# Kernel optimization log

Measured on AMD Instinct MI355X. Metric: run time of the kernel, lower is better.

Reference implementation:

```python
import jax, jax.numpy as jnp
import numpy as np

STEPS = 4
EMB = 128
HEADS = 3
NUM_GRAPHS = 64
NODES_PER = 64
N = NUM_GRAPHS * NODES_PER
E_SPARSE = N * 16
DATA_LENS = [NODES_PER] * NUM_GRAPHS


def _complete_edge_index(data_lens):
    # dense_to_sparse(complete_matrix) -> all (i,j) pairs within each block,
    # including self loops (diagonal of complete_matrix is 1).
    srcs, dsts = [], []
    start = 0
    for l in data_lens:
        idx = np.arange(start, start + l)
        srcs.append(np.repeat(idx, l))
        dsts.append(np.tile(idx, l))
        start += l
    return np.stack([np.concatenate(srcs), np.concatenate(dsts)]).astype(np.int32)


def leaky(x, slope=0.01):
    return jnp.where(x >= 0, x, slope * x)


def setup_inputs() -> dict:
    key = jax.random.key(0)
    ks = jax.random.split(key, 16)
    s = 0.05
    edge_complete = jnp.asarray(_complete_edge_index(DATA_LENS))
    # sparse edge_index: random edges within each graph
    src_local = jax.random.randint(ks[1], (E_SPARSE,), 0, NODES_PER)
    dst_local = jax.random.randint(ks[2], (E_SPARSE,), 0, NODES_PER)
    gid = jnp.repeat(jnp.arange(NUM_GRAPHS), E_SPARSE // NUM_GRAPHS) * NODES_PER
    edge_index = jnp.stack([src_local + gid, dst_local + gid]).astype(jnp.int32)
    batch_ind = jnp.repeat(jnp.arange(NUM_GRAPHS), NODES_PER).astype(jnp.int32)
    return {
        "x": jax.random.normal(ks[0], (N, EMB), jnp.float32),
        "edge_index": edge_index,
        "batch_ind": batch_ind,
        "edge_complete": edge_complete,
        "Wm": jax.random.normal(ks[3], (STEPS, EMB, EMB)) * s,
        "bm": jnp.zeros((STEPS, EMB)),
        "Wa": jax.random.normal(ks[4], (STEPS, 3 * EMB, EMB)) * s,
        "ba": jnp.zeros((STEPS, EMB)),
        "Wl": jax.random.normal(ks[5], (STEPS - 1, EMB, HEADS * EMB)) * s,
        "bl": jnp.zeros((STEPS - 1, HEADS * EMB)),
        "Wr": jax.random.normal(ks[6], (STEPS - 1, EMB, HEADS * EMB)) * s,
        "br": jnp.zeros((STEPS - 1, HEADS * EMB)),
        "att_w": jax.random.normal(ks[7], (STEPS - 1, HEADS, EMB)) * s,
        "att_bias": jnp.zeros((STEPS - 1, EMB)),
    }


def _graphnet(x, x_att, batch_ind, src, dst, Wm, bm, Wa, ba):
    # message: f_mess(x_j)  (edge_attr is None in this model)
    m = leaky(x[src] @ Wm + bm)                               # [E, D]
    agg = jax.ops.segment_max(m, dst, num_segments=x.shape[0])
    agg = jnp.where(jnp.isneginf(agg), 0.0, agg)              # PyG fills empty with 0
    xg = x_att[batch_ind]                                     # [N, D]
    z = jnp.concatenate([x, xg, agg], axis=1)                 # [N, 3D]
    return leaky(z @ Wa + ba) + x


def _gatv2(x, src, dst, Wl, bl, Wr, br, att, bias):
    n = x.shape[0]
    xl = (x @ Wl + bl).reshape(n, HEADS, EMB)                 # source transform
    xr = (x @ Wr + br).reshape(n, HEADS, EMB)                 # target transform
    e = leaky(xl[src] + xr[dst], 0.2)                         # [E, H, D]
    logits = jnp.einsum('ehd,hd->eh', e, att)                 # [E, H]
    mx = jax.ops.segment_max(logits, dst, num_segments=n)
    mx = jnp.where(jnp.isneginf(mx), 0.0, mx)
    alpha = jnp.exp(logits - mx[dst])
    denom = jax.ops.segment_sum(alpha, dst, num_segments=n)
    alpha = alpha / denom[dst]                                # softmax over incoming edges
    out = jax.ops.segment_sum(alpha[:, :, None] * xl[src], dst, num_segments=n)
    return out.mean(axis=1) + bias                            # concat=False -> head mean


def reference(x, edge_index, batch_ind, edge_complete, Wm, bm, Wa, ba, Wl, bl, Wr, br, att_w, att_bias):
    src, dst = edge_index[0], edge_index[1]
    csrc, cdst = edge_complete[0], edge_complete[1]
    x_att = jnp.zeros((NUM_GRAPHS, EMB), x.dtype)
    for i in range(STEPS):
        x = _graphnet(x, x_att, batch_ind, src, dst, Wm[i], bm[i], Wa[i], ba[i])
        if i < STEPS - 1:
            x_att_nodes = leaky(_gatv2(x, csrc, cdst, Wl[i], bl[i], Wr[i], br[i], att_w[i], att_bias[i]))
            # original indexes xg = x_att[batch_ind]; x_att here is per-node, so
            # emulate torch semantics: x_att has len(x) rows, indexed by batch_ind.
            x_att = x_att_nodes
        # note: in original, x_att has shape [len(x), emb]; xg = x_att[batch_ind]
    return x


if __name__ == "__main__":
    out = reference(**setup_inputs())
    print(out.shape)
```

## Files before the change

kernel.cpp:

```cpp
#include <hip/hip_runtime.h>
#include <math.h>

#define D 128
#define GB 64
#define BT 512
#define ZP 264
#define XLP 72

typedef __attribute__((ext_vector_type(8))) short bf16x8;
typedef __attribute__((ext_vector_type(4))) float f32x4;
typedef __attribute__((ext_vector_type(4))) unsigned u32x4;

__device__ __forceinline__ float leaky01(float v) { return v >= 0.f ? v : 0.01f * v; }
__device__ __forceinline__ unsigned short f2bf(float f) {
    unsigned u = __float_as_uint(f);
    u += 0x7FFFu + ((u >> 16) & 1u);
    return (unsigned short)(u >> 16);
}
__device__ __forceinline__ float bf2f(unsigned short s) {
    return __uint_as_float(((unsigned)s) << 16);
}

__device__ __forceinline__ void st_sys_u32(unsigned* p, unsigned v) {
    asm volatile("global_store_dword %0, %1, off sc0 sc1" :: "v"(p), "v"(v) : "memory");
}
__device__ __forceinline__ void st_sys_u128(unsigned* p, u32x4 v) {
    asm volatile("global_store_dwordx4 %0, %1, off sc0 sc1" :: "v"(p), "v"(v) : "memory");
}
__device__ __forceinline__ unsigned ld_sys_u32(const unsigned* p) {
    unsigned v;
    asm volatile("global_load_dword %0, %1, off sc0 sc1\n\ts_waitcnt vmcnt(0)"
                 : "=v"(v) : "v"(p) : "memory");
    return v;
}
__device__ __forceinline__ u32x4 ld_sys_u128(const unsigned* p) {
    u32x4 v;
    asm volatile("global_load_dwordx4 %0, %1, off sc0 sc1\n\ts_waitcnt vmcnt(0)"
                 : "=v"(v) : "v"(p) : "memory");
    return v;
}
__device__ __forceinline__ void waitst() { asm volatile("s_waitcnt vmcnt(0)" ::: "memory"); }

__global__ void k_wconv(const float* __restrict__ Wm, const float* __restrict__ Wa,
                        const float* __restrict__ Wl,
                        unsigned short* __restrict__ Wmt, unsigned short* __restrict__ Wat,
                        unsigned short* __restrict__ Wlt,
                        unsigned* __restrict__ flags) {
    int gid = blockIdx.x * blockDim.x + threadIdx.x;
    if (blockIdx.x == 0 && threadIdx.x < 8) st_sys_u32(&flags[threadIdx.x], 0u);
    if (gid < 16384) {
        int o = gid * 4;
        int s = o >> 14, rem = o & 16383, n = rem >> 7, k0 = rem & 127;
        const float* src = Wm + (size_t)s * 16384;
        unsigned short* dst = Wmt + o;
#pragma unroll
        for (int j = 0; j < 4; ++j) dst[j] = f2bf(src[(size_t)(k0 + j) * 128 + n]);
    } else if (gid < 49152) {
        int o = (gid - 16384) * 4;
        int s = o >> 15, rem = o & 32767, n = rem >> 8, k0 = rem & 255;
        int row = (k0 < 128) ? k0 : (k0 + 128);
        const float* src = Wa + (size_t)s * 49152;
        unsigned short* dst = Wat + o;
#pragma unroll
        for (int j = 0; j < 4; ++j) dst[j] = f2bf(src[(size_t)(row + j) * 128 + n]);
    } else if (gid < 86016) {
        int o = (gid - 49152) * 4;
        int s = o / 49152, rem = o % 49152, n = rem >> 7, k0 = rem & 127;
        const float* src = Wl + (size_t)s * 49152;
        unsigned short* dst = Wlt + o;
#pragma unroll
        for (int j = 0; j < 4; ++j) dst[j] = f2bf(src[(size_t)(k0 + j) * 384 + n]);
    }
}

struct Args {
    const float* x0;
    const int* e_src; const int* e_dst;
    const unsigned short *Wmt, *Wat, *Wlt;
    const float *Wa, *Wr, *bm, *ba, *bl, *br, *att_w, *att_bias;
    unsigned short* xg0;
    unsigned* flagX;
    float* out;
};

__global__ __launch_bounds__(BT) void k_mega(Args p) {
    const int tid = threadIdx.x, bid = blockIdx.x, g = bid;
    const int wave = tid >> 6, lane = tid & 63;
    const int m16 = lane & 15, kg = lane >> 4;
    const int col = wave * 16 + m16;

    __shared__ unsigned short zsb[64][ZP];
    __shared__ unsigned short hs[64][128];
    __shared__ unsigned mlo[64], mhi[64];
    __shared__ float att_s[3][D];
    __shared__ float xgrow[D];
    __shared__ float ygmid[D];
    __shared__ float red[512];
    __shared__ float alpha_s[64];
    __shared__ float accO_s[D];

    unsigned short (*xl_h)[XLP] = (unsigned short(*)[XLP])&zsb[0][0];
    unsigned short (*xg_s)[128] = (unsigned short(*)[128])&hs[0][0];

    if (tid < 64) { mlo[tid] = 0u; mhi[tid] = 0u; }
    __syncthreads();
    {
        int i0 = g * 1024 + tid;
        int s1 = p.e_src[i0] - g * 64,       d1 = p.e_dst[i0] - g * 64;
        int s2 = p.e_src[i0 + 512] - g * 64, d2 = p.e_dst[i0 + 512] - g * 64;
        atomicOr(s1 < 32 ? &mlo[d1] : &mhi[d1], 1u << (s1 & 31));
        atomicOr(s2 < 32 ? &mlo[d2] : &mhi[d2], 1u << (s2 & 31));
    }

    float xreg[16];
    {
        const float* xp = p.x0 + (size_t)g * 64 * D;
#pragma unroll
        for (int mt = 0; mt < 4; ++mt)
#pragma unroll
            for (int r = 0; r < 4; ++r) xreg[mt * 4 + r] = xp[(mt * 16 + kg * 4 + r) * D + col];
    }
    __syncthreads();

    for (int step = 0; step < 4; ++step) {
#pragma unroll
        for (int mt = 0; mt < 4; ++mt)
#pragma unroll
            for (int r = 0; r < 4; ++r) zsb[mt * 16 + kg * 4 + r][col] = f2bf(xreg[mt * 4 + r]);
        if (step < 3 && tid < 384) att_s[tid >> 7][tid & 127] = p.att_w[step * 384 + tid];
        __syncthreads();

        {
            const unsigned short* Wb = p.Wmt + ((size_t)(step * 128 + col) * 128 + kg * 8);
            bf16x8 bB[4];
#pragma unroll
            for (int kt = 0; kt < 4; ++kt) bB[kt] = *(const bf16x8*)(Wb + kt * 32);
            float bb = p.bm[step * 128 + col];
#pragma unroll
            for (int mt = 0; mt < 4; ++mt) {
                f32x4 acc = {0.f, 0.f, 0.f, 0.f};
#pragma unroll
                for (int kt = 0; kt < 4; ++kt) {
                    bf16x8 a = *(const bf16x8*)&zsb[mt * 16 + m16][kt * 32 + kg * 8];
                    acc = __builtin_amdgcn_mfma_f32_16x16x32_bf16(a, bB[kt], acc, 0, 0, 0);
                }
#pragma unroll
                for (int r = 0; r < 4; ++r)
                    hs[mt * 16 + kg * 4 + r][col] = f2bf(leaky01(acc[r] + bb));
            }
        }
        __syncthreads();

        {
            int r0 = wave * 8;
            unsigned lo[8], hi[8];
#pragma unroll
            for (int r = 0; r < 8; ++r) {
                lo[r] = (unsigned)__builtin_amdgcn_readfirstlane((int)mlo[r0 + r]);
                hi[r] = (unsigned)__builtin_amdgcn_readfirstlane((int)mhi[r0 + r]);
            }
            float m0[8], m1[8];
#pragma unroll
            for (int r = 0; r < 8; ++r) { m0[r] = -INFINITY; m1[r] = -INFINITY; }
#pragma unroll 4
            for (int s = 0; s < 32; ++s) {
                unsigned hv = *(const unsigned*)&hs[s][lane * 2];
                float v0 = bf2f((unsigned short)(hv & 0xffffu));
                float v1 = bf2f((unsigned short)(hv >> 16));
#pragma unroll
                for (int r = 0; r < 8; ++r)
                    if ((lo[r] >> s) & 1u) { m0[r] = fmaxf(m0[r], v0); m1[r] = fmaxf(m1[r], v1); }
            }
#pragma unroll 4
            for (int s = 32; s < 64; ++s) {
                unsigned hv = *(const unsigned*)&hs[s][lane * 2];
                float v0 = bf2f((unsigned short)(hv & 0xffffu));
                float v1 = bf2f((unsigned short)(hv >> 16));
#pragma unroll
                for (int r = 0; r < 8; ++r)
                    if ((hi[r] >> (s - 32)) & 1u) { m0[r] = fmaxf(m0[r], v0); m1[r] = fmaxf(m1[r], v1); }
            }
#pragma unroll
            for (int r = 0; r < 8; ++r) {
                unsigned pk = (lo[r] | hi[r])
                                  ? (((unsigned)f2bf(m1[r]) << 16) | (unsigned)f2bf(m0[r]))
                                  : 0u;
                *(unsigned*)&zsb[r0 + r][128 + lane * 2] = pk;
            }
        }

        if (step > 0) {
            int n = tid & 127, q = tid >> 7;
            float a = 0.f;
            const float* Wmid = p.Wa + (size_t)step * 49152 + (size_t)(128 + q * 32) * 128 + n;
#pragma unroll 8
            for (int k2 = 0; k2 < 32; ++k2) a += xgrow[q * 32 + k2] * Wmid[(size_t)k2 * 128];
            red[q * 128 + n] = a;
            __syncthreads();
            if (tid < 128) ygmid[tid] = red[tid] + red[128 + tid] + red[256 + tid] + red[384 + tid];
        }
        __syncthreads();

        {
            const unsigned short* Wb = p.Wat + ((size_t)(step * 128 + col) * 256 + kg * 8);
            bf16x8 bB[8];
#pragma unroll
            for (int kt = 0; kt < 8; ++kt) bB[kt] = *(const bf16x8*)(Wb + kt * 32);
            float extra = p.ba[step * 128 + col] + (step > 0 ? ygmid[col] : 0.f);
#pragma unroll
            for (int mt = 0; mt < 4; ++mt) {
                f32x4 acc = {0.f, 0.f, 0.f, 0.f};
#pragma unroll
                for (int kt = 0; kt < 8; ++kt) {
                    bf16x8 a = *(const bf16x8*)&zsb[mt * 16 + m16][kt * 32 + kg * 8];
                    acc = __builtin_amdgcn_mfma_f32_16x16x32_bf16(a, bB[kt], acc, 0, 0, 0);
                }
#pragma unroll
                for (int r = 0; r < 4; ++r) {
                    float v = leaky01(acc[r] + extra) + xreg[mt * 4 + r];
                    xreg[mt * 4 + r] = v;
                    if (step == 3) p.out[((size_t)g * 64 + mt * 16 + kg * 4 + r) * D + col] = v;
                }
            }
        }

        if (step < 3) {
            __syncthreads();
            unsigned short* xg0g = p.xg0 + (size_t)step * 8192;
            if (bid == 0) {
#pragma unroll
                for (int mt = 0; mt < 4; ++mt)
#pragma unroll
                    for (int r = 0; r < 4; ++r) {
                        int row = mt * 16 + kg * 4 + r;
                        unsigned off = (unsigned)(row * 256 + col * 2) ^ (unsigned)((row & 7) << 4);
                        *(unsigned short*)((char*)&xg_s[0][0] + off) = f2bf(xreg[mt * 4 + r]);
                    }
                __syncthreads();
                for (int j = tid; j < 1024; j += BT) {
                    unsigned boff = (unsigned)(j * 16);
                    int row = j >> 4;
                    u32x4 v = *(u32x4*)((char*)&xg_s[0][0] + (boff ^ ((row & 7) << 4)));
                    st_sys_u128((unsigned*)((char*)xg0g + boff), v);
                }
                waitst();
                __syncthreads();
                if (tid == 0) st_sys_u32(p.flagX + step, 1u);
            } else {
                if (tid == 0) {
                    int it = 0;
                    while (ld_sys_u32(p.flagX + step) == 0 && it++ < (1 << 22))
                        __builtin_amdgcn_s_sleep(2);
                }
                __syncthreads();
                for (int j = tid; j < 1024; j += BT) {
                    unsigned boff = (unsigned)(j * 16);
                    int row = j >> 4;
                    u32x4 v = ld_sys_u128((const unsigned*)((const char*)xg0g + boff));
                    *(u32x4*)((char*)&xg_s[0][0] + (boff ^ ((row & 7) << 4))) = v;
                }
                __syncthreads();
            }

            float* xr_g = ygmid;
            for (int h = 0; h < 3; ++h) {
                {
                    const unsigned short* Wb = p.Wlt + ((size_t)(step * 384 + h * 128 + col) * 128 + kg * 8);
                    bf16x8 bB[4];
#pragma unroll
                    for (int kt = 0; kt < 4; ++kt) bB[kt] = *(const bf16x8*)(Wb + kt * 32);
                    float bb = p.bl[step * 384 + h * 128 + col];
#pragma unroll
                    for (int mt = 0; mt < 4; ++mt) {
                        f32x4 acc = {0.f, 0.f, 0.f, 0.f};
#pragma unroll
                        for (int kt = 0; kt < 4; ++kt) {
                            int row = mt * 16 + m16;
                            unsigned off = (unsigned)(row * 256 + (kt * 32 + kg * 8) * 2) ^ (unsigned)((row & 7) << 4);
                            bf16x8 a = *(const bf16x8*)((const char*)&xg_s[0][0] + off);
                            acc = __builtin_amdgcn_mfma_f32_16x16x32_bf16(a, bB[kt], acc, 0, 0, 0);
                        }
                        int s0 = mt * 16 + kg * 4;
                        unsigned pk0 = (unsigned)f2bf(acc[0] + bb) | ((unsigned)f2bf(acc[1] + bb) << 16);
                        unsigned pk1 = (unsigned)f2bf(acc[2] + bb) | ((unsigned)f2bf(acc[3] + bb) << 16);
                        *(unsigned*)&xl_h[col][s0] = pk0;
                        *(unsigned*)&xl_h[col][s0 + 2] = pk1;
                    }
                }
                {
                    int n = tid & 127, q = tid >> 7;
                    float a = 0.f;
                    const float* Wrp = p.Wr + (size_t)step * 49152 + (size_t)(q * 32) * 384 + h * 128 + n;
#pragma unroll 8
                    for (int k2 = 0; k2 < 32; ++k2) {
                        int k = q * 32 + k2;
                        unsigned b = ((unsigned)(g * 256 + k * 2)) ^ (unsigned)((g & 7) << 4);
                        float xv = bf2f(*(const unsigned short*)((const char*)&xg_s[0][0] + b));
                        a += xv * Wrp[(size_t)k2 * 384];
                    }
                    red[q * 128 + n] = a;
                }
                __syncthreads();
                if (tid < 128)
                    xr_g[tid] = red[tid] + red[128 + tid] + red[256 + tid] + red[384 + tid]
                                + p.br[step * 384 + h * 128 + tid];
                __syncthreads();
                {
                    float part = 0.f;
                    int kb = wave * 16;
#pragma unroll
                    for (int kk = 0; kk < 16; ++kk) {
                        int k = kb + kk;
                        float t = bf2f(xl_h[k][lane]) + xr_g[k];
                        t = (t >= 0.f) ? t : 0.2f * t;
                        part += att_s[h][k] * t;
                    }
                    red[wave * 64 + lane] = part;
                }
                __syncthreads();
                if (wave == 0) {
                    float lg = 0.f;
#pragma unroll
                    for (int w2 = 0; w2 < 8; ++w2) lg += red[w2 * 64 + lane];
                    float mx = lg;
#pragma unroll
                    for (int o = 32; o > 0; o >>= 1) mx = fmaxf(mx, __shfl_xor(mx, o));
                    float a = __expf(lg - mx), sm = a;
#pragma unroll
                    for (int o = 32; o > 0; o >>= 1) sm += __shfl_xor(sm, o);
                    alpha_s[lane] = a / sm;
                }
                __syncthreads();
                {
                    int c = tid & 127, q = tid >> 7;
                    float pv = 0.f;
#pragma unroll
                    for (int s2 = 0; s2 < 16; ++s2) {
                        int s = q * 16 + s2;
                        pv += alpha_s[s] * bf2f(xl_h[c][s]);
                    }
                    red[q * 128 + c] = pv;
                }
                __syncthreads();
                if (tid < 128) {
                    float s4 = red[tid] + red[128 + tid] + red[256 + tid] + red[384 + tid];
                    accO_s[tid] = (h == 0) ? s4 : accO_s[tid] + s4;
                }
                __syncthreads();
            }
            if (tid < 128)
                xgrow[tid] = leaky01(accO_s[tid] * (1.f / 3.f) + p.att_bias[step * 128 + tid]);
        }
        __syncthreads();
    }
}

extern "C" void kernel_launch(void* const* d_in, const int* in_sizes, int n_in,
                              void* d_out, int out_size, void* d_ws, size_t ws_size,
                              hipStream_t stream) {
    (void)n_in; (void)out_size; (void)ws_size;
    const float* x_in     = (const float*)d_in[0];
    const int*   edge_idx = (const int*)d_in[1];
    const float* Wm  = (const float*)d_in[4];
    const float* bm  = (const float*)d_in[5];
    const float* Wa  = (const float*)d_in[6];
    const float* ba  = (const float*)d_in[7];
    const float* Wl  = (const float*)d_in[8];
    const float* bl  = (const float*)d_in[9];
    const float* Wr  = (const float*)d_in[10];
    const float* br  = (const float*)d_in[11];
    const float* att_w    = (const float*)d_in[12];
    const float* att_bias = (const float*)d_in[13];
    const int E = in_sizes[1] / 2;

    char* ws = (char*)d_ws;
    size_t off = 0;
    auto alloc = [&](size_t bytes) { void* pp = ws + off; off += (bytes + 255) & ~size_t(255); return pp; };
    unsigned short* xg0 = (unsigned short*)alloc((size_t)3 * 64 * 128 * 2);
    unsigned short* Wmt = (unsigned short*)alloc((size_t)4 * 128 * 128 * 2);
    unsigned short* Wat = (unsigned short*)alloc((size_t)4 * 128 * 256 * 2);
    unsigned short* Wlt = (unsigned short*)alloc((size_t)3 * 384 * 128 * 2);
    unsigned* flags     = (unsigned*)alloc(8 * 4);

    k_wconv<<<336, 256, 0, stream>>>(Wm, Wa, Wl, Wmt, Wat, Wlt, flags);

    Args a;
    a.x0 = x_in;
    a.e_src = edge_idx;
    a.e_dst = edge_idx + E;
    a.Wmt = Wmt; a.Wat = Wat; a.Wlt = Wlt;
    a.Wa = Wa; a.Wr = Wr; a.bm = bm; a.ba = ba; a.bl = bl; a.br = br;
    a.att_w = att_w; a.att_bias = att_bias;
    a.xg0 = xg0; a.flagX = flags;
    a.out = (float*)d_out;
    void* kargs[] = { (void*)&a };
    (void)hipLaunchCooperativeKernel((void*)k_mega, dim3(GB), dim3(BT), kargs, 0, stream);
}
```

Before: 146.6 us.

## Double block to 1024 threads and batch GATv2 heads to cut barriers

Result: no change. 147.1 us (+0.4%).

```diff
diff --git a/kernel.cpp b/kernel.cpp
--- a/kernel.cpp
+++ b/kernel.cpp
@@ -3,9 +3,9 @@
 
 #define D 128
 #define GB 64
-#define BT 512
+#define BT 1024
 #define ZP 264
-#define XLP 72
+#define XLP 74
 
 typedef __attribute__((ext_vector_type(8))) short bf16x8;
 typedef __attribute__((ext_vector_type(4))) float f32x4;
@@ -87,46 +87,51 @@
     const int tid = threadIdx.x, bid = blockIdx.x, g = bid;
     const int wave = tid >> 6, lane = tid & 63;
     const int m16 = lane & 15, kg = lane >> 4;
-    const int col = wave * 16 + m16;
+    const int wtile = wave >> 1;
+    const int half = wave & 1;
+    const int col = wtile * 16 + m16;
 
     __shared__ unsigned short zsb[64][ZP];
     __shared__ unsigned short hs[64][128];
+    __shared__ unsigned short xl3[3][128][XLP];
+    __shared__ float red[3072];
     __shared__ unsigned mlo[64], mhi[64];
     __shared__ float att_s[3][D];
     __shared__ float xgrow[D];
     __shared__ float ygmid[D];
-    __shared__ float red[512];
-    __shared__ float alpha_s[64];
-    __shared__ float accO_s[D];
-
-    unsigned short (*xl_h)[XLP] = (unsigned short(*)[XLP])&zsb[0][0];
+    __shared__ float xr3[384];
+    __shared__ float alpha3[192];
+
     unsigned short (*xg_s)[128] = (unsigned short(*)[128])&hs[0][0];
 
     if (tid < 64) { mlo[tid] = 0u; mhi[tid] = 0u; }
     __syncthreads();
     {
         int i0 = g * 1024 + tid;
-        int s1 = p.e_src[i0] - g * 64,       d1 = p.e_dst[i0] - g * 64;
-        int s2 = p.e_src[i0 + 512] - g * 64, d2 = p.e_dst[i0 + 512] - g * 64;
+        int s1 = p.e_src[i0] - g * 64, d1 = p.e_dst[i0] - g * 64;
         atomicOr(s1 < 32 ? &mlo[d1] : &mhi[d1], 1u << (s1 & 31));
-        atomicOr(s2 < 32 ? &mlo[d2] : &mhi[d2], 1u << (s2 & 31));
     }
 
-    float xreg[16];
+    float xreg[8];
     {
         const float* xp = p.x0 + (size_t)g * 64 * D;
 #pragma unroll
-        for (int mt = 0; mt < 4; ++mt)
-#pragma unroll
-            for (int r = 0; r < 4; ++r) xreg[mt * 4 + r] = xp[(mt * 16 + kg * 4 + r) * D + col];
+        for (int i = 0; i < 2; ++i) {
+            int mt = half * 2 + i;
+#pragma unroll
+            for (int r = 0; r < 4; ++r)
+                xreg[i * 4 + r] = xp[(mt * 16 + kg * 4 + r) * D + col];
+        }
     }
     __syncthreads();
 
     for (int step = 0; step < 4; ++step) {
 #pragma unroll
-        for (int mt = 0; mt < 4; ++mt)
-#pragma unroll
-            for (int r = 0; r < 4; ++r) zsb[mt * 16 + kg * 4 + r][col] = f2bf(xreg[mt * 4 + r]);
+        for (int i = 0; i < 2; ++i) {
+            int mt = half * 2 + i;
+#pragma unroll
+            for (int r = 0; r < 4; ++r) zsb[mt * 16 + kg * 4 + r][col] = f2bf(xreg[i * 4 + r]);
+        }
         if (step < 3 && tid < 384) att_s[tid >> 7][tid & 127] = p.att_w[step * 384 + tid];
         __syncthreads();
 
@@ -137,7 +142,8 @@
             for (int kt = 0; kt < 4; ++kt) bB[kt] = *(const bf16x8*)(Wb + kt * 32);
             float bb = p.bm[step * 128 + col];
 #pragma unroll
-            for (int mt = 0; mt < 4; ++mt) {
+            for (int i = 0; i < 2; ++i) {
+                int mt = half * 2 + i;
                 f32x4 acc = {0.f, 0.f, 0.f, 0.f};
 #pragma unroll
                 for (int kt = 0; kt < 4; ++kt) {
@@ -152,23 +158,23 @@
         __syncthreads();
 
         {
-            int r0 = wave * 8;
-            unsigned lo[8], hi[8];
-#pragma unroll
-            for (int r = 0; r < 8; ++r) {
+            int r0 = wave * 4;
+            unsigned lo[4], hi[4];
+#pragma unroll
+            for (int r = 0; r < 4; ++r) {
                 lo[r] = (unsigned)__builtin_amdgcn_readfirstlane((int)mlo[r0 + r]);
                 hi[r] = (unsigned)__builtin_amdgcn_readfirstlane((int)mhi[r0 + r]);
             }
-            float m0[8], m1[8];
-#pragma unroll
-            for (int r = 0; r < 8; ++r) { m0[r] = -INFINITY; m1[r] = -INFINITY; }
+            float m0[4], m1[4];
+#pragma unroll
+            for (int r = 0; r < 4; ++r) { m0[r] = -INFINITY; m1[r] = -INFINITY; }
 #pragma unroll 4
             for (int s = 0; s < 32; ++s) {
                 unsigned hv = *(const unsigned*)&hs[s][lane * 2];
                 float v0 = bf2f((unsigned short)(hv & 0xffffu));
                 float v1 = bf2f((unsigned short)(hv >> 16));
 #pragma unroll
-                for (int r = 0; r < 8; ++r)
+                for (int r = 0; r < 4; ++r)
                     if ((lo[r] >> s) & 1u) { m0[r] = fmaxf(m0[r], v0); m1[r] = fmaxf(m1[r], v1); }
             }
 #pragma unroll 4
@@ -177,11 +183,11 @@
                 float v0 = bf2f((unsigned short)(hv & 0xffffu));
                 float v1 = bf2f((unsigned short)(hv >> 16));
 #pragma unroll
-                for (int r = 0; r < 8; ++r)
+                for (int r = 0; r < 4; ++r)
                     if ((hi[r] >> (s - 32)) & 1u) { m0[r] = fmaxf(m0[r], v0); m1[r] = fmaxf(m1[r], v1); }
             }
 #pragma unroll
-            for (int r = 0; r < 8; ++r) {
+            for (int r = 0; r < 4; ++r) {
                 unsigned pk = (lo[r] | hi[r])
                                   ? (((unsigned)f2bf(m1[r]) << 16) | (unsigned)f2bf(m0[r]))
                                   : 0u;
@@ -192,12 +198,17 @@
         if (step > 0) {
             int n = tid & 127, q = tid >> 7;
             float a = 0.f;
-            const float* Wmid = p.Wa + (size_t)step * 49152 + (size_t)(128 + q * 32) * 128 + n;
+            const float* Wmid = p.Wa + (size_t)step * 49152 + (size_t)(128 + q * 16) * 128 + n;
 #pragma unroll 8
-            for (int k2 = 0; k2 < 32; ++k2) a += xgrow[q * 32 + k2] * Wmid[(size_t)k2 * 128];
+            for (int k2 = 0; k2 < 16; ++k2) a += xgrow[q * 16 + k2] * Wmid[(size_t)k2 * 128];
             red[q * 128 + n] = a;
             __syncthreads();
-            if (tid < 128) ygmid[tid] = red[tid] + red[128 + tid] + red[256 + tid] + red[384 + tid];
+            if (tid < 128) {
+                float s8 = 0.f;
+#pragma unroll
+                for (int q2 = 0; q2 < 8; ++q2) s8 += red[q2 * 128 + tid];
+                ygmid[tid] = s8;
+            }
         }
         __syncthreads();
 
@@ -208,7 +219,8 @@
             for (int kt = 0; kt < 8; ++kt) bB[kt] = *(const bf16x8*)(Wb + kt * 32);
             float extra = p.ba[step * 128 + col] + (step > 0 ? ygmid[col] : 0.f);
 #pragma unroll
-            for (int mt = 0; mt < 4; ++mt) {
+            for (int i = 0; i < 2; ++i) {
+                int mt = half * 2 + i;
                 f32x4 acc = {0.f, 0.f, 0.f, 0.f};
 #pragma unroll
                 for (int kt = 0; kt < 8; ++kt) {
@@ -217,8 +229,8 @@
                 }
 #pragma unroll
                 for (int r = 0; r < 4; ++r) {
-                    float v = leaky01(acc[r] + extra) + xreg[mt * 4 + r];
-                    xreg[mt * 4 + r] = v;
+                    float v = leaky01(acc[r] + extra) + xreg[i * 4 + r];
+                    xreg[i * 4 + r] = v;
                     if (step == 3) p.out[((size_t)g * 64 + mt * 16 + kg * 4 + r) * D + col] = v;
                 }
             }
@@ -229,18 +241,20 @@
             unsigned short* xg0g = p.xg0 + (size_t)step * 8192;
             if (bid == 0) {
 #pragma unroll
-                for (int mt = 0; mt < 4; ++mt)
+                for (int i = 0; i < 2; ++i) {
+                    int mt = half * 2 + i;
 #pragma unroll
                     for (int r = 0; r < 4; ++r) {
                         int row = mt * 16 + kg * 4 + r;
                         unsigned off = (unsigned)(row * 256 + col * 2) ^ (unsigned)((row & 7) << 4);
-                        *(unsigned short*)((char*)&xg_s[0][0] + off) = f2bf(xreg[mt * 4 + r]);
+                        *(unsigned short*)((char*)&xg_s[0][0] + off) = f2bf(xreg[i * 4 + r]);
                     }
+                }
                 __syncthreads();
-                for (int j = tid; j < 1024; j += BT) {
-                    unsigned boff = (unsigned)(j * 16);
-                    int row = j >> 4;
-                    u32x4 v = *(u32x4*)((char*)&xg_s[0][0] + (boff ^ ((row & 7) << 4)));
+                {
+                    unsigned boff = (unsigned)tid * 16;
+                    int row = tid >> 4;
+                    u32x4 v = *(u32x4*)((char*)&xg_s[0][0] + (boff ^ (unsigned)((row & 7) << 4)));
                     st_sys_u128((unsigned*)((char*)xg0g + boff), v);
                 }
                 waitst();
@@ -253,103 +267,108 @@
                         __builtin_amdgcn_s_sleep(2);
                 }
                 __syncthreads();
-                for (int j = tid; j < 1024; j += BT) {
-                    unsigned boff = (unsigned)(j * 16);
-                    int row = j >> 4;
+                {
+                    unsigned boff = (unsigned)tid * 16;
+                    int row = tid >> 4;
                     u32x4 v = ld_sys_u128((const unsigned*)((const char*)xg0g + boff));
-                    *(u32x4*)((char*)&xg_s[0][0] + (boff ^ ((row & 7) << 4))) = v;
+                    *(u32x4*)((char*)&xg_s[0][0] + (boff ^ (unsigned)((row & 7) << 4))) = v;
                 }
                 __syncthreads();
             }
 
-            float* xr_g = ygmid;
             for (int h = 0; h < 3; ++h) {
-                {
-                    const unsigned short* Wb = p.Wlt + ((size_t)(step * 384 + h * 128 + col) * 128 + kg * 8);
-                    bf16x8 bB[4];
-#pragma unroll
-                    for (int kt = 0; kt < 4; ++kt) bB[kt] = *(const bf16x8*)(Wb + kt * 32);
-                    float bb = p.bl[step * 384 + h * 128 + col];
-#pragma unroll
-                    for (int mt = 0; mt < 4; ++mt) {
-                        f32x4 acc = {0.f, 0.f, 0.f, 0.f};
-#pragma unroll
-                        for (int kt = 0; kt < 4; ++kt) {
-                            int row = mt * 16 + m16;
-                            unsigned off = (unsigned)(row * 256 + (kt * 32 + kg * 8) * 2) ^ (unsigned)((row & 7) << 4);
-                            bf16x8 a = *(const bf16x8*)((const char*)&xg_s[0][0] + off);
-                            acc = __builtin_amdgcn_mfma_f32_16x16x32_bf16(a, bB[kt], acc, 0, 0, 0);
-                        }
-                        int s0 = mt * 16 + kg * 4;
-                        unsigned pk0 = (unsigned)f2bf(acc[0] + bb) | ((unsigned)f2bf(acc[1] + bb) << 16);
-                        unsigned pk1 = (unsigned)f2bf(acc[2] + bb) | ((unsigned)f2bf(acc[3] + bb) << 16);
-                        *(unsigned*)&xl_h[col][s0] = pk0;
-                        *(unsigned*)&xl_h[col][s0 + 2] = pk1;
+                const unsigned short* Wb = p.Wlt + ((size_t)(step * 384 + h * 128 + col) * 128 + kg * 8);
+                bf16x8 bB[4];
+#pragma unroll
+                for (int kt = 0; kt < 4; ++kt) bB[kt] = *(const bf16x8*)(Wb + kt * 32);
+                float bb = p.bl[step * 384 + h * 128 + col];
+#pragma unroll
+                for (int i = 0; i < 2; ++i) {
+                    int mt = half * 2 + i;
+                    f32x4 acc = {0.f, 0.f, 0.f, 0.f};
+#pragma unroll
+                    for (int kt = 0; kt < 4; ++kt) {
+                        int row = mt * 16 + m16;
+                        unsigned off = (unsigned)(row * 256 + (kt * 32 + kg * 8) * 2) ^ (unsigned)((row & 7) << 4);
+                        bf16x8 a = *(const bf16x8*)((const char*)&xg_s[0][0] + off);
+                        acc = __builtin_amdgcn_mfma_f32_16x16x32_bf16(a, bB[kt], acc, 0, 0, 0);
                     }
-                }
-                {
-                    int n = tid & 127, q = tid >> 7;
-                    float a = 0.f;
-                    const float* Wrp = p.Wr + (size_t)step * 49152 + (size_t)(q * 32) * 384 + h * 128 + n;
+                    int s0 = mt * 16 + kg * 4;
+                    unsigned pk0 = (unsigned)f2bf(acc[0] + bb) | ((unsigned)f2bf(acc[1] + bb) << 16);
+                    unsigned pk1 = (unsigned)f2bf(acc[2] + bb) | ((unsigned)f2bf(acc[3] + bb) << 16);
+                    *(unsigned*)&xl3[h][col][s0] = pk0;
+                    *(unsigned*)&xl3[h][col][s0 + 2] = pk1;
+                }
+            }
+            if (tid < 768) {
+                int q = (tid >= 384) ? 1 : 0;
+                int n3 = tid - q * 384;
+                int h = n3 >> 7, n = n3 & 127;
+                float a = 0.f;
+                const float* Wrp = p.Wr + (size_t)step * 49152 + (size_t)(q * 64) * 384 + h * 128 + n;
 #pragma unroll 8
-                    for (int k2 = 0; k2 < 32; ++k2) {
-                        int k = q * 32 + k2;
-                        unsigned b = ((unsigned)(g * 256 + k * 2)) ^ (unsigned)((g & 7) << 4);
-                        float xv = bf2f(*(const unsigned short*)((const char*)&xg_s[0][0] + b));
-                        a += xv * Wrp[(size_t)k2 * 384];
-                    }
-                    red[q * 128 + n] = a;
-                }
-                __syncthreads();
-                if (tid < 128)
-                    xr_g[tid] = red[tid] + red[128 + tid] + red[256 + tid] + red[384 + tid]
-                                + p.br[step * 384 + h * 128 + tid];
-                __syncthreads();
-                {
+                for (int k2 = 0; k2 < 64; ++k2) {
+                    int k = q * 64 + k2;
+                    unsigned b = ((unsigned)(g * 256 + k * 2)) ^ (unsigned)((g & 7) << 4);
+                    float xv = bf2f(*(const unsigned short*)((const char*)&xg_s[0][0] + b));
+                    a += xv * Wrp[(size_t)k2 * 384];
+                }
+                red[q * 384 + n3] = a;
+            }
+            __syncthreads();
+            if (tid < 384) xr3[tid] = red[tid] + red[384 + tid] + p.br[step * 384 + tid];
+            __syncthreads();
+
+            {
+                int kb = wave * 8;
+#pragma unroll
+                for (int h = 0; h < 3; ++h) {
                     float part = 0.f;
-                    int kb = wave * 16;
-#pragma unroll
-                    for (int kk = 0; kk < 16; ++kk) {
+#pragma unroll
+                    for (int kk = 0; kk < 8; ++kk) {
                         int k = kb + kk;
-                        float t = bf2f(xl_h[k][lane]) + xr_g[k];
+                        float t = bf2f(xl3[h][k][lane]) + xr3[h * 128 + k];
                         t = (t >= 0.f) ? t : 0.2f * t;
                         part += att_s[h][k] * t;
                     }
-                    red[wave * 64 + lane] = part;
-                }
-                __syncthreads();
-                if (wave == 0) {
-                    float lg = 0.f;
-#pragma unroll
-                    for (int w2 = 0; w2 < 8; ++w2) lg += red[w2 * 64 + lane];
-                    float mx = lg;
-#pragma unroll
-                    for (int o = 32; o > 0; o >>= 1) mx = fmaxf(mx, __shfl_xor(mx, o));
-                    float a = __expf(lg - mx), sm = a;
-#pragma unroll
-                    for (int o = 32; o > 0; o >>= 1) sm += __shfl_xor(sm, o);
-                    alpha_s[lane] = a / sm;
-                }
-                __syncthreads();
-                {
-                    int c = tid & 127, q = tid >> 7;
+                    red[(h * 16 + wave) * 64 + lane] = part;
+                }
+            }
+            __syncthreads();
+            if (tid < 192) {
+                int h = tid >> 6;
+                float lg = 0.f;
+#pragma unroll
+                for (int w2 = 0; w2 < 16; ++w2) lg += red[(h * 16 + w2) * 64 + lane];
+                float mx = lg;
+#pragma unroll
+                for (int o = 32; o > 0; o >>= 1) mx = fmaxf(mx, __shfl_xor(mx, o));
+                float a = __expf(lg - mx), sm = a;
+#pragma unroll
+                for (int o = 32; o > 0; o >>= 1) sm += __shfl_xor(sm, o);
+                alpha3[h * 64 + lane] = a / sm;
+            }
+            __syncthreads();
+
+            {
+                int c = tid & 127, q = tid >> 7;
+                if (q < 6) {
+                    int h = q >> 1, sq = q & 1;
                     float pv = 0.f;
 #pragma unroll
-                    for (int s2 = 0; s2 < 16; ++s2) {
-                        int s = q * 16 + s2;
-                        pv += alpha_s[s] * bf2f(xl_h[c][s]);
+                    for (int s2 = 0; s2 < 32; ++s2) {
+                        int s = sq * 32 + s2;
+                        pv += alpha3[h * 64 + s] * bf2f(xl3[h][c][s]);
                     }
                     red[q * 128 + c] = pv;
                 }
-                __syncthreads();
-                if (tid < 128) {
-                    float s4 = red[tid] + red[128 + tid] + red[256 + tid] + red[384 + tid];
-                    accO_s[tid] = (h == 0) ? s4 : accO_s[tid] + s4;
-                }
-                __syncthreads();
-            }
-            if (tid < 128)
-                xgrow[tid] = leaky01(accO_s[tid] * (1.f / 3.f) + p.att_bias[step * 128 + tid]);
+            }
+            __syncthreads();
+            if (tid < 128) {
+                float accO = red[tid] + red[128 + tid] + red[256 + tid]
+                           + red[384 + tid] + red[512 + tid] + red[640 + tid];
+                xgrow[tid] = leaky01(accO * (1.f / 3.f) + p.att_bias[step * 128 + tid]);
+            }
         }
         __syncthreads();
     }
```
